# Kernel optimization log

Hardware: AMD Instinct MI355X
Metric: run time of the kernel (lower is better)

Reference implementation:

```python
import jax, jax.numpy as jnp
import numpy as np

B, N, G, H = 64, 1000, 500, 256
TANH_CLIP = 10.0


def setup_inputs() -> dict:
    key = jax.random.key(0)
    ks = jax.random.split(key, 8)
    embeddings = jax.random.normal(ks[0], (B, N, H), dtype=jnp.float32)
    dists = jax.random.uniform(ks[1], (B, N, N), dtype=jnp.float32)
    last_node = jax.random.randint(ks[2], (B, G), 0, N)
    visited = jax.random.uniform(ks[3], (B, G, N)) < 0.3
    group_ninf_mask = jnp.where(visited, -jnp.inf, 0.0).astype(jnp.float32)
    s = 1.0 / np.sqrt(H)
    Wq_graph = jax.random.normal(ks[4], (H, H), dtype=jnp.float32) * s
    Wq_first = jax.random.normal(ks[5], (H, H), dtype=jnp.float32) * s
    Wq_last = jax.random.normal(ks[6], (H, H), dtype=jnp.float32) * s
    W_visited = jax.random.normal(ks[7], (H, H), dtype=jnp.float32) * s
    return dict(embeddings=embeddings, dists=dists, last_node=last_node,
                group_ninf_mask=group_ninf_mask, Wq_graph=Wq_graph,
                Wq_first=Wq_first, Wq_last=Wq_last, W_visited=W_visited)


def reference(embeddings, dists, last_node, group_ninf_mask,
              Wq_graph, Wq_first, Wq_last, W_visited) -> jnp.ndarray:
    b, n, h = embeddings.shape
    g = last_node.shape[1]
    inv_sqrt_h = 1.0 / np.float32(np.sqrt(h))
    inv_sqrt_2 = np.float32(1.0 / np.sqrt(2.0))

    # reset(): graph query from mean-pooled embeddings  [B,1,H]
    q_graph = jnp.einsum('bih,oh->bio', embeddings.mean(axis=1, keepdims=True), Wq_graph)

    # gather last-node embeddings  [B,G,H]
    idx = jnp.broadcast_to(last_node[:, :, None], (b, g, h))
    last_emb = jnp.take_along_axis(embeddings, idx, axis=1)
    q_last = jnp.einsum('bgh,oh->bgo', last_emb, Wq_last)
    # first call: q_first built from the same last-node embedding
    q_first = jnp.einsum('bgh,oh->bgo', last_emb, Wq_first)

    # visited-set query: mask (-inf->1) @ embeddings / N, then linear
    mask_visited = jnp.where(jnp.isneginf(group_ninf_mask), 1.0, group_ninf_mask)
    pooled = jnp.einsum('bgn,bnh->bgh', mask_visited, embeddings) / np.float32(n)
    q_visited = jnp.einsum('bgh,oh->bgo', pooled, W_visited)

    # distances from last node to all nodes  [B,G,N]
    didx = jnp.broadcast_to(last_node[:, :, None], (b, g, n))
    distances = jnp.take_along_axis(dists, didx, axis=1)

    final_q = q_last + q_first + q_graph + q_visited  # [B,G,H]
    score = jnp.einsum('bgh,bnh->bgn', final_q, embeddings) * inv_sqrt_h - distances * inv_sqrt_2
    score_clipped = TANH_CLIP * jnp.tanh(score)
    mask_prob = jnp.where(jnp.isneginf(group_ninf_mask), -1e8, group_ninf_mask)
    return jax.nn.softmax(score_clipped + mask_prob, axis=-1)
```

## Files before the change

kernel.cpp:

```cpp
#include <hip/hip_runtime.h>
#include <hip/hip_fp16.h>
#include <math.h>

#define Bb 64
#define Nn 1000
#define Gg 500
#define Hh 256
#define GP 512
#define NP 1024

#define WS_MP   0u
#define WS_QG   16384u
#define WS_RS   32768u
#define WS_BM   65536u
#define WS_WC16 1114112u
#define WS_E16  1179648u
#define WS_T16  9371648u
#define WS_P16  17760256u
#define WS_F16  WS_T16
#define WS_PO   21954560u

typedef __attribute__((ext_vector_type(8))) short short8;
typedef __attribute__((ext_vector_type(8))) _Float16 f16x8;
typedef __attribute__((ext_vector_type(4))) float f32x4;
typedef __attribute__((ext_vector_type(4))) unsigned short u16x4;

#define MFMAH(a,b,c) __builtin_amdgcn_mfma_f32_16x16x32_f16(a,b,c,0,0,0)
#define SW(row, chunk) (((row) << 6) + ((((chunk) ^ ((row) & 7))) << 3))

__device__ __forceinline__ unsigned short f16b(float v) {
  return __half_as_ushort(__float2half(v));
}

__global__ __launch_bounds__(256) void k_zero(float* __restrict__ ws) {
  int bid = blockIdx.x, t = threadIdx.x;
  if (bid < 64) ws[WS_MP + bid * 256 + t] = 0.f;
  else          ws[WS_RS + (bid - 64) * 256 + t] = 0.f;
}

__global__ __launch_bounds__(256) void k_prep(const float* __restrict__ emb,
                                              float* __restrict__ ws) {
  __shared__ float tile[64][65];
  __shared__ float csumL[256];
  int nt = blockIdx.x, ht = blockIdx.y, b = blockIdx.z;
  int t = threadIdx.x, c = t & 63, w = t >> 6;
  int n0 = nt * 64, h0 = ht * 64;
  unsigned short* e16 = (unsigned short*)(ws + WS_E16);
  unsigned short* t16 = (unsigned short*)(ws + WS_T16);
  float csum = 0.f;
#pragma unroll
  for (int rr = 0; rr < 16; ++rr) {
    int r = w * 16 + rr;
    int n = n0 + r;
    float v = 0.f;
    if (n < Nn) {
      size_t idx = ((size_t)(b * Nn + n)) * Hh + h0 + c;
      v = emb[idx];
      e16[idx] = f16b(v);
    }
    tile[r][c] = v;
    csum += v;
  }
  __syncthreads();
  {
    int h_l = t >> 2, nseg = t & 3;
    short8 h8a, h8b;
#pragma unroll
    for (int i = 0; i < 16; ++i) {
      float v = tile[nseg * 16 + i][h_l];
      unsigned short hv = f16b(v);
      if (i < 8) h8a[i] = (short)hv;
      else       h8b[i-8] = (short)hv;
    }
    size_t base = ((size_t)(b * Hh + h0 + h_l)) * NP + n0 + nseg * 16;
    *(short8*)(t16 + base) = h8a; *(short8*)(t16 + base + 8) = h8b;
  }
  __syncthreads();
  csumL[t] = csum;
  __syncthreads();
  if (t < 64) {
    float s = csumL[t] + csumL[t+64] + csumL[t+128] + csumL[t+192];
    atomicAdd(ws + WS_MP + b * Hh + h0 + t, s);
  }
}

__global__ __launch_bounds__(256) void k_qgraph(const float* __restrict__ Wg,
                                                float* __restrict__ ws) {
  __shared__ float mean[Hh];
  int b = blockIdx.x, t = threadIdx.x;
  mean[t] = ws[WS_MP + b*Hh + t] * (1.0f/Nn);
  __syncthreads();
  const float4* wrow = (const float4*)(Wg + (size_t)t * Hh);
  float acc = 0.f;
#pragma unroll
  for (int h4 = 0; h4 < Hh/4; ++h4) {
    float4 w = wrow[h4];
    acc += mean[h4*4]*w.x + mean[h4*4+1]*w.y + mean[h4*4+2]*w.z + mean[h4*4+3]*w.w;
  }
  ws[WS_QG + b*Hh + t] = acc;
}

__global__ __launch_bounds__(256) void k_wcat(const float* __restrict__ Wf,
                                              const float* __restrict__ Wl,
                                              const float* __restrict__ Wv,
                                              float* __restrict__ ws) {
  int o = blockIdx.x, k = threadIdx.x;
  unsigned short* wc = (unsigned short*)(ws + WS_WC16);
  wc[o*512 + k]       = f16b(Wv[o*Hh + k]);
  wc[o*512 + 256 + k] = f16b(Wl[o*Hh + k] + Wf[o*Hh + k]);
}

__global__ __launch_bounds__(256) void k_bm(const float* __restrict__ gm,
                                            float* __restrict__ ws) {
  int w = threadIdx.x >> 6, l = threadIdx.x & 63;
  int row = blockIdx.x * 4 + w;
  int b = row >> 9, g = row & 511;
  unsigned long long* dst = (unsigned long long*)((unsigned short*)(ws + WS_BM) + (size_t)row * 64);
  if (g < Gg) {
    const float* src = gm + ((size_t)b * Gg + g) * Nn;
#pragma unroll
    for (int i = 0; i < 16; ++i) {
      int n = i * 64 + l;
      bool bit = (n < Nn) ? (src[n] < -1e30f) : false;
      unsigned long long m = __ballot(bit);
      if (l == i) dst[i] = m;
    }
  } else {
    if (l < 16) dst[l] = 0ull;
  }
}

__global__ __launch_bounds__(256, 2) void k_pool(float* __restrict__ ws) {
  __shared__ __align__(16) unsigned short sT[128*64];
  int ht = blockIdx.x, gt = blockIdx.y, b = blockIdx.z;
  int t = threadIdx.x, w = t >> 6, lane = t & 63;
  int wh = w >> 1, wg = w & 1, l15 = lane & 15, lk = lane >> 4;
  const unsigned short* t16 = (const unsigned short*)(ws + WS_T16);
  const unsigned short* bmp = (const unsigned short*)(ws + WS_BM);
  unsigned short* p16 = (unsigned short*)(ws + WS_P16);
  int h0 = ht*128, g0 = gt*128;
  f32x4 acc[4][4] = {};
  const unsigned short* brow[4];
#pragma unroll
  for (int fn = 0; fn < 4; ++fn) {
    int g = g0 + wg*64 + fn*16 + l15; if (g > Gg-1) g = Gg-1;
    brow[fn] = bmp + ((size_t)(b*GP + g)) * 64;
  }
  int bitoff = (lk & 1) * 8;
  int srow = t >> 1, sc0 = (t & 1) * 4;
  size_t sbase = ((size_t)(b*Hh + h0 + srow)) * NP;
  for (int st = 0; st < 16; ++st) {
    int k0 = st * 64;
#pragma unroll
    for (int i = 0; i < 4; ++i) {
      int cc = sc0 + i;
      *(short8*)&sT[SW(srow, cc)] = *(const short8*)(t16 + sbase + k0 + cc*8);
    }
    __syncthreads();
#pragma unroll
    for (int kk = 0; kk < 64; kk += 32) {
      f16x8 ah[4], bmf[4];
#pragma unroll
      for (int fm = 0; fm < 4; ++fm)
        ah[fm] = *(const f16x8*)&sT[SW(wh*64 + fm*16 + l15, (kk>>3) + lk)];
#pragma unroll
      for (int fn = 0; fn < 4; ++fn) {
        unsigned c = brow[fn][((k0 + kk) >> 4) + (lk >> 1)];
        short8 bs;
#pragma unroll
        for (int i = 0; i < 8; ++i)
          bs[i] = ((c >> (bitoff + i)) & 1) ? (short)0x3C00 : (short)0;
        bmf[fn] = *(const f16x8*)&bs;
      }
#pragma unroll
      for (int fm = 0; fm < 4; ++fm)
#pragma unroll
        for (int fn = 0; fn < 4; ++fn)
          acc[fm][fn] = MFMAH(ah[fm], bmf[fn], acc[fm][fn]);
    }
    __syncthreads();
  }
#pragma unroll
  for (int fm = 0; fm < 4; ++fm)
#pragma unroll
    for (int fn = 0; fn < 4; ++fn) {
      int h = h0 + wh*64 + fm*16 + lk*4;
      int g = g0 + wg*64 + fn*16 + l15;
      u16x4 v4;
#pragma unroll
      for (int j = 0; j < 4; ++j) v4[j] = f16b(acc[fm][fn][j] * (1.0f/Nn));
      *(u16x4*)(p16 + ((size_t)(b*GP + g)) * Hh + h) = v4;
    }
}

__global__ __launch_bounds__(256, 2) void k_finalq(const int* __restrict__ last_node,
                                                   float* __restrict__ ws) {
  __shared__ __align__(16) unsigned short sA[128*64], sB[128*64];
  __shared__ int lL[128];
  int ot = blockIdx.x, gt = blockIdx.y, b = blockIdx.z;
  int t = threadIdx.x, w = t >> 6, lane = t & 63;
  int wo = w >> 1, wg = w & 1, l15 = lane & 15, lk = lane >> 4;
  const unsigned short* wc = (const unsigned short*)(ws + WS_WC16);
  const unsigned short* p16 = (const unsigned short*)(ws + WS_P16);
  const unsigned short* e16 = (const unsigned short*)(ws + WS_E16);
  unsigned short* f16 = (unsigned short*)(ws + WS_F16);
  int o0 = ot*128, g0 = gt*128;
  if (t < 128) lL[t] = last_node[b*Gg + ((g0 + t) < Gg ? (g0 + t) : Gg-1)];
  __syncthreads();
  f32x4 acc[4][4] = {};
  int srow = t >> 1, sc0 = (t & 1) * 4;
  size_t abase = ((size_t)(o0 + srow)) * 512;
  size_t pbase = ((size_t)(b*GP + g0 + srow)) * Hh;
  size_t lbase = ((size_t)(b*Nn + lL[srow])) * Hh;
  for (int st = 0; st < 8; ++st) {
    int k0 = st * 64;
#pragma unroll
    for (int i = 0; i < 4; ++i) {
      int cc = sc0 + i;
      int d = SW(srow, cc);
      *(short8*)&sA[d] = *(const short8*)(wc + abase + k0 + cc*8);
      if (k0 < 256)
        *(short8*)&sB[d] = *(const short8*)(p16 + pbase + k0 + cc*8);
      else
        *(short8*)&sB[d] = *(const short8*)(e16 + lbase + (k0 - 256) + cc*8);
    }
    __syncthreads();
#pragma unroll
    for (int kk = 0; kk < 64; kk += 32) {
      f16x8 a[4], bb[4];
#pragma unroll
      for (int fm = 0; fm < 4; ++fm)
        a[fm] = *(const f16x8*)&sA[SW(wo*64 + fm*16 + l15, (kk>>3) + lk)];
#pragma unroll
      for (int fn = 0; fn < 4; ++fn)
        bb[fn] = *(const f16x8*)&sB[SW(wg*64 + fn*16 + l15, (kk>>3) + lk)];
#pragma unroll
      for (int fm = 0; fm < 4; ++fm)
#pragma unroll
        for (int fn = 0; fn < 4; ++fn)
          acc[fm][fn] = MFMAH(a[fm], bb[fn], acc[fm][fn]);
    }
    __syncthreads();
  }
#pragma unroll
  for (int fm = 0; fm < 4; ++fm) {
    int o = o0 + wo*64 + fm*16 + lk*4;
    float4 qv = *(const float4*)(ws + WS_QG + b*Hh + o);
    float q4[4] = {qv.x, qv.y, qv.z, qv.w};
#pragma unroll
    for (int fn = 0; fn < 4; ++fn) {
      int g = g0 + wg*64 + fn*16 + l15;
      u16x4 v4;
#pragma unroll
      for (int j = 0; j < 4; ++j) v4[j] = f16b(acc[fm][fn][j] + q4[j]);
      *(u16x4*)(f16 + ((size_t)(b*GP + g)) * Hh + o) = v4;
    }
  }
}

__global__ __launch_bounds__(256, 4) void k_score(const float* __restrict__ dists,
                                                  const int* __restrict__ last_node,
                                                  float* __restrict__ ws) {
  __shared__ __align__(16) unsigned short sE[128*64], sF[128*64];
  __shared__ int lL[128];
  int nt = blockIdx.x, gt = blockIdx.y, b = blockIdx.z;
  int t = threadIdx.x, w = t >> 6, lane = t & 63;
  int wn = w >> 1, wg = w & 1, l15 = lane & 15, lk = lane >> 4;
  const unsigned short* e16 = (const unsigned short*)(ws + WS_E16);
  const unsigned short* f16 = (const unsigned short*)(ws + WS_F16);
  const unsigned short* bmp = (const unsigned short*)(ws + WS_BM);
  unsigned short* po = (unsigned short*)(ws + WS_PO);
  float* rs = ws + WS_RS;
  int n0 = nt*128, g0 = gt*128;
  if (t < 128) lL[t] = last_node[b*Gg + ((g0 + t) < Gg ? (g0 + t) : Gg-1)];
  __syncthreads();
  f32x4 acc[4][4] = {};
  int srow = t >> 1, sc0 = (t & 1) * 4;
  int nr = n0 + srow; if (nr > Nn-1) nr = Nn-1;
  size_t ebase = ((size_t)(b*Nn + nr)) * Hh;
  size_t fbase = ((size_t)(b*GP + g0 + srow)) * Hh;
  for (int st = 0; st < 4; ++st) {
    int k0 = st * 64;
#pragma unroll
    for (int i = 0; i < 4; ++i) {
      int cc = sc0 + i;
      int d = SW(srow, cc);
      *(short8*)&sE[d] = *(const short8*)(e16 + ebase + k0 + cc*8);
      *(short8*)&sF[d] = *(const short8*)(f16 + fbase + k0 + cc*8);
    }
    __syncthreads();
#pragma unroll
    for (int kk = 0; kk < 64; kk += 32) {
      f16x8 a[4], bb[4];
#pragma unroll
      for (int fm = 0; fm < 4; ++fm)
        a[fm] = *(const f16x8*)&sE[SW(wn*64 + fm*16 + l15, (kk>>3) + lk)];
#pragma unroll
      for (int fn = 0; fn < 4; ++fn)
        bb[fn] = *(const f16x8*)&sF[SW(wg*64 + fn*16 + l15, (kk>>3) + lk)];
#pragma unroll
      for (int fm = 0; fm < 4; ++fm)
#pragma unroll
        for (int fn = 0; fn < 4; ++fn)
          acc[fm][fn] = MFMAH(a[fm], bb[fn], acc[fm][fn]);
    }
    __syncthreads();
  }
  const float c2 = 0.70710678118654752f;
  float rsum[4] = {0.f, 0.f, 0.f, 0.f};
#pragma unroll
  for (int fn = 0; fn < 4; ++fn) {
    int gl = wg*64 + fn*16 + l15;
    int g = g0 + gl;
    if (g < Gg) {
      int L = lL[gl];
      const float* drow = dists + ((size_t)(b*Nn + L)) * Nn;
      const unsigned short* bmr = bmp + ((size_t)(b*GP + g)) * 64;
      unsigned short* prow = po + ((size_t)(b*Gg + g)) * 1024;
#pragma unroll
      for (int fm = 0; fm < 4; ++fm) {
        int n = n0 + wn*64 + fm*16 + lk*4;
        if (n < Nn) {
          float4 d4 = *(const float4*)(drow + n);
          unsigned cb = bmr[n >> 4];
          int bo = n & 15;
          float dd[4] = {d4.x, d4.y, d4.z, d4.w};
          unsigned short h4[4];
#pragma unroll
          for (int j = 0; j < 4; ++j) {
            float s = fmaf(acc[fm][fn][j], 0.0625f, -dd[j] * c2);
            float e = __expf(-2.0f * fabsf(s));
            float r = __builtin_amdgcn_rcpf(1.0f + e);
            float m = fmaf(-20.0f, e * r, 10.0f);
            float parg = copysignf(m, s) - 10.0f;
            float p = ((cb >> (bo + j)) & 1) ? 0.f : __expf(parg);
            rsum[fn] += p;
            h4[j] = f16b(p);
          }
          uint2 u = { (unsigned)h4[0] | ((unsigned)h4[1] << 16),
                      (unsigned)h4[2] | ((unsigned)h4[3] << 16) };
          *(uint2*)(prow + n) = u;
        }
      }
    }
  }
#pragma unroll
  for (int fn = 0; fn < 4; ++fn) {
    rsum[fn] += __shfl_xor(rsum[fn], 16);
    rsum[fn] += __shfl_xor(rsum[fn], 32);
    int g = g0 + wg*64 + fn*16 + l15;
    if (lk == 0 && g < Gg) atomicAdd(rs + b*GP + g, rsum[fn]);
  }
}

__global__ __launch_bounds__(256) void k_norm(const float* __restrict__ ws,
                                              float* __restrict__ out) {
  int idx = blockIdx.x * 256 + threadIdx.x;
  int bg = idx / 250;
  int n = (idx - bg * 250) * 4;
  int b = bg / Gg, g = bg - b * Gg;
  const unsigned short* po = (const unsigned short*)(ws + WS_PO);
  float inv = 1.0f / ws[WS_RS + b*GP + g];
  uint2 u = *(const uint2*)(po + (size_t)bg * 1024 + n);
  float4 o4;
  o4.x = __half2float(__ushort_as_half((unsigned short)(u.x & 0xFFFF))) * inv;
  o4.y = __half2float(__ushort_as_half((unsigned short)(u.x >> 16))) * inv;
  o4.z = __half2float(__ushort_as_half((unsigned short)(u.y & 0xFFFF))) * inv;
  o4.w = __half2float(__ushort_as_half((unsigned short)(u.y >> 16))) * inv;
  *(float4*)(out + (size_t)bg * Nn + n) = o4;
}

extern "C" void kernel_launch(void* const* d_in, const int* in_sizes, int n_in,
                              void* d_out, int out_size, void* d_ws, size_t ws_size,
                              hipStream_t stream) {
  const float* emb       = (const float*)d_in[0];
  const float* dists     = (const float*)d_in[1];
  const int*   last_node = (const int*)d_in[2];
  const float* gm        = (const float*)d_in[3];
  const float* Wg        = (const float*)d_in[4];
  const float* Wf        = (const float*)d_in[5];
  const float* Wl        = (const float*)d_in[6];
  const float* Wv        = (const float*)d_in[7];
  float* out = (float*)d_out;
  float* ws  = (float*)d_ws;

  hipLaunchKernelGGL(k_zero,   dim3(192),       dim3(256), 0, stream, ws);
  hipLaunchKernelGGL(k_prep,   dim3(16,4,Bb),   dim3(256), 0, stream, emb, ws);
  hipLaunchKernelGGL(k_qgraph, dim3(Bb),        dim3(256), 0, stream, Wg, ws);
  hipLaunchKernelGGL(k_wcat,   dim3(256),       dim3(256), 0, stream, Wf, Wl, Wv, ws);
  hipLaunchKernelGGL(k_bm,     dim3(Bb*GP/4),   dim3(256), 0, stream, gm, ws);
  hipLaunchKernelGGL(k_pool,   dim3(2,4,Bb),    dim3(256), 0, stream, ws);
  hipLaunchKernelGGL(k_finalq, dim3(2,4,Bb),    dim3(256), 0, stream, last_node, ws);
  hipLaunchKernelGGL(k_score,  dim3(8,4,Bb),    dim3(256), 0, stream, dists, last_node, ws);
  hipLaunchKernelGGL(k_norm,   dim3(31250),     dim3(256), 0, stream, ws, out);
}
```

Baseline: 326.9 us.

## Vectorize prep and norm memory accesses, reorder score grid to group by n-tile

k_prep now loads and stores with float4 and u16x4 per thread and reduces column sums through a 16x64 shared array, which removes one barrier pair. k_norm handles 8 outputs per thread with a 16-byte load and two float4 stores, halving the grid size. k_score swaps its grid axes so the g-tile varies fastest, so consecutive blocks reuse the same embedding n-tile and dists rows in cache. These are several unrelated memory-efficiency tweaks, and the grid reorder could change L2 locality either way.

Result: no change. 321.3 us (-1.7%).

```diff
diff --git a/kernel.cpp b/kernel.cpp
--- a/kernel.cpp
+++ b/kernel.cpp
@@ -40,27 +40,31 @@
 
 __global__ __launch_bounds__(256) void k_prep(const float* __restrict__ emb,
                                               float* __restrict__ ws) {
-  __shared__ float tile[64][65];
-  __shared__ float csumL[256];
+  __shared__ float tile[64][68];
+  __shared__ float colsum[16][64];
   int nt = blockIdx.x, ht = blockIdx.y, b = blockIdx.z;
-  int t = threadIdx.x, c = t & 63, w = t >> 6;
+  int t = threadIdx.x;
+  int c4 = (t & 15) * 4, r0 = t >> 4;
   int n0 = nt * 64, h0 = ht * 64;
   unsigned short* e16 = (unsigned short*)(ws + WS_E16);
   unsigned short* t16 = (unsigned short*)(ws + WS_T16);
-  float csum = 0.f;
-#pragma unroll
-  for (int rr = 0; rr < 16; ++rr) {
-    int r = w * 16 + rr;
+  float cs0 = 0.f, cs1 = 0.f, cs2 = 0.f, cs3 = 0.f;
+#pragma unroll
+  for (int rr = 0; rr < 4; ++rr) {
+    int r = r0 + rr * 16;
     int n = n0 + r;
-    float v = 0.f;
+    float4 v = {0.f, 0.f, 0.f, 0.f};
     if (n < Nn) {
-      size_t idx = ((size_t)(b * Nn + n)) * Hh + h0 + c;
-      v = emb[idx];
-      e16[idx] = f16b(v);
-    }
-    tile[r][c] = v;
-    csum += v;
-  }
+      size_t idx = ((size_t)(b * Nn + n)) * Hh + h0 + c4;
+      v = *(const float4*)(emb + idx);
+      u16x4 e4 = { f16b(v.x), f16b(v.y), f16b(v.z), f16b(v.w) };
+      *(u16x4*)(e16 + idx) = e4;
+    }
+    *(float4*)&tile[r][c4] = v;
+    cs0 += v.x; cs1 += v.y; cs2 += v.z; cs3 += v.w;
+  }
+  colsum[r0][c4 + 0] = cs0; colsum[r0][c4 + 1] = cs1;
+  colsum[r0][c4 + 2] = cs2; colsum[r0][c4 + 3] = cs3;
   __syncthreads();
   {
     int h_l = t >> 2, nseg = t & 3;
@@ -75,11 +79,10 @@
     size_t base = ((size_t)(b * Hh + h0 + h_l)) * NP + n0 + nseg * 16;
     *(short8*)(t16 + base) = h8a; *(short8*)(t16 + base + 8) = h8b;
   }
-  __syncthreads();
-  csumL[t] = csum;
-  __syncthreads();
   if (t < 64) {
-    float s = csumL[t] + csumL[t+64] + csumL[t+128] + csumL[t+192];
+    float s = 0.f;
+#pragma unroll
+    for (int i = 0; i < 16; ++i) s += colsum[i][t];
     atomicAdd(ws + WS_MP + b * Hh + h0 + t, s);
   }
 }
@@ -263,7 +266,7 @@
                                                   float* __restrict__ ws) {
   __shared__ __align__(16) unsigned short sE[128*64], sF[128*64];
   __shared__ int lL[128];
-  int nt = blockIdx.x, gt = blockIdx.y, b = blockIdx.z;
+  int gt = blockIdx.x, nt = blockIdx.y, b = blockIdx.z;
   int t = threadIdx.x, w = t >> 6, lane = t & 63;
   int wn = w >> 1, wg = w & 1, l15 = lane & 15, lk = lane >> 4;
   const unsigned short* e16 = (const unsigned short*)(ws + WS_E16);
@@ -356,18 +359,24 @@
 __global__ __launch_bounds__(256) void k_norm(const float* __restrict__ ws,
                                               float* __restrict__ out) {
   int idx = blockIdx.x * 256 + threadIdx.x;
-  int bg = idx / 250;
-  int n = (idx - bg * 250) * 4;
+  int bg = idx / 125;
+  int n = (idx - bg * 125) * 8;
   int b = bg / Gg, g = bg - b * Gg;
   const unsigned short* po = (const unsigned short*)(ws + WS_PO);
   float inv = 1.0f / ws[WS_RS + b*GP + g];
-  uint2 u = *(const uint2*)(po + (size_t)bg * 1024 + n);
-  float4 o4;
-  o4.x = __half2float(__ushort_as_half((unsigned short)(u.x & 0xFFFF))) * inv;
-  o4.y = __half2float(__ushort_as_half((unsigned short)(u.x >> 16))) * inv;
-  o4.z = __half2float(__ushort_as_half((unsigned short)(u.y & 0xFFFF))) * inv;
-  o4.w = __half2float(__ushort_as_half((unsigned short)(u.y >> 16))) * inv;
-  *(float4*)(out + (size_t)bg * Nn + n) = o4;
+  uint4 u = *(const uint4*)(po + (size_t)bg * 1024 + n);
+  float* orow = out + (size_t)bg * Nn + n;
+  float4 o0, o1;
+  o0.x = __half2float(__ushort_as_half((unsigned short)(u.x & 0xFFFF))) * inv;
+  o0.y = __half2float(__ushort_as_half((unsigned short)(u.x >> 16))) * inv;
+  o0.z = __half2float(__ushort_as_half((unsigned short)(u.y & 0xFFFF))) * inv;
+  o0.w = __half2float(__ushort_as_half((unsigned short)(u.y >> 16))) * inv;
+  o1.x = __half2float(__ushort_as_half((unsigned short)(u.z & 0xFFFF))) * inv;
+  o1.y = __half2float(__ushort_as_half((unsigned short)(u.z >> 16))) * inv;
+  o1.z = __half2float(__ushort_as_half((unsigned short)(u.w & 0xFFFF))) * inv;
+  o1.w = __half2float(__ushort_as_half((unsigned short)(u.w >> 16))) * inv;
+  *(float4*)orow = o0;
+  *(float4*)(orow + 4) = o1;
 }
 
 extern "C" void kernel_launch(void* const* d_in, const int* in_sizes, int n_in,
@@ -391,6 +400,6 @@
   hipLaunchKernelGGL(k_bm,     dim3(Bb*GP/4),   dim3(256), 0, stream, gm, ws);
   hipLaunchKernelGGL(k_pool,   dim3(2,4,Bb),    dim3(256), 0, stream, ws);
   hipLaunchKernelGGL(k_finalq, dim3(2,4,Bb),    dim3(256), 0, stream, last_node, ws);
-  hipLaunchKernelGGL(k_score,  dim3(8,4,Bb),    dim3(256), 0, stream, dists, last_node, ws);
-  hipLaunchKernelGGL(k_norm,   dim3(31250),     dim3(256), 0, stream, ws, out);
-}
+  hipLaunchKernelGGL(k_score,  dim3(4,8,Bb),    dim3(256), 0, stream, dists, last_node, ws);
+  hipLaunchKernelGGL(k_norm,   dim3(15625),     dim3(256), 0, stream, ws, out);
+}
```
